# Performance work log

Hardware: AMD Instinct MI355X
Metric: run time of the kernel (lower is better)

Reference implementation:

```python
import jax, jax.numpy as jnp
import numpy as np
import math

B, T, EMB, HD = 4, 2048, 2048, 128
HALF = HD // 2


def setup_inputs() -> dict:
    key = jax.random.key(0)
    ks = jax.random.split(key, 4)
    x = jax.random.normal(ks[0], (B, T, EMB), dtype=jnp.float32)
    s = 1.0 / math.sqrt(EMB)
    Wq = jax.random.normal(ks[1], (EMB, HD), dtype=jnp.float32) * s
    Wk = jax.random.normal(ks[2], (EMB, HD), dtype=jnp.float32) * s
    Wv = jax.random.normal(ks[3], (EMB, HD), dtype=jnp.float32) * s
    # Standard RoPE rotation table: theta_i = 10000^(-2i/HD), angle = pos * theta
    inv_freq = 1.0 / (10000.0 ** (np.arange(0, HALF, dtype=np.float32) / HALF))
    angles = np.arange(T, dtype=np.float32)[:, None] * inv_freq[None, :]  # [T, HALF]
    rot_cos = jnp.asarray(np.cos(angles), dtype=jnp.float32)
    rot_sin = jnp.asarray(np.sin(angles), dtype=jnp.float32)
    # Additive causal mask: 0 on/below diagonal, -1e9 above
    NEG = -1e9
    mask = jnp.where(jnp.tril(jnp.ones((T, T), dtype=bool)), 0.0, NEG).astype(jnp.float32)
    return {"x": x, "Wq": Wq, "Wk": Wk, "Wv": Wv,
            "rot_cos": rot_cos, "rot_sin": rot_sin, "mask": mask}


def _apply_rope(q, rot_cos, rot_sin):
    # q: [B, T, HD]; view last dim as HALF complex pairs and rotate
    qp = q.reshape(q.shape[0], q.shape[1], HALF, 2)
    re, im = qp[..., 0], qp[..., 1]
    out_re = re * rot_cos - im * rot_sin  # broadcast [T,HALF] over batch
    out_im = re * rot_sin + im * rot_cos
    return jnp.stack([out_re, out_im], axis=-1).reshape(q.shape)


def reference(x, Wq, Wk, Wv, rot_cos, rot_sin, mask):
    Q = x @ Wq  # [B, T, HD]
    K = x @ Wk
    V = x @ Wv
    Q = _apply_rope(Q, rot_cos, rot_sin)
    K = _apply_rope(K, rot_cos, rot_sin)
    scores = jnp.einsum('bqd,bkd->bqk', Q, K) / math.sqrt(HD)
    probs = jax.nn.softmax(scores + mask, axis=-1)  # dropout is identity in eval
    return jnp.einsum('bqk,bkd->bqd', probs, V)
```

## Files before the change

kernel.cpp:

```cpp
#include <hip/hip_runtime.h>
#include <cstddef>
#include <cstdint>

#define T_SEQ 2048
#define EMB_D 2048
#define HD_D  128

typedef __attribute__((ext_vector_type(8))) short short8;
typedef __attribute__((ext_vector_type(4))) float f32x4;
typedef __attribute__((ext_vector_type(4))) unsigned short ushort4v;
typedef __attribute__((ext_vector_type(8))) unsigned short ushort8v;
typedef __attribute__((ext_vector_type(2))) unsigned int uint2v;

static __device__ __forceinline__ unsigned short f2bf_rne(float f) {
    union { float f; unsigned u; } v; v.f = f;
    unsigned r = v.u + 0x7fffu + ((v.u >> 16) & 1u);
    return (unsigned short)(r >> 16);
}
static __device__ __forceinline__ unsigned short f2bf_fast(float f) {
    union { float f; unsigned u; } v; v.f = f;
    return (unsigned short)((v.u + 0x8000u) >> 16);
}
static __device__ __forceinline__ float bf2f(unsigned short h) {
    union { unsigned u; float f; } v; v.u = ((unsigned)h) << 16;
    return v.f;
}
static __device__ __forceinline__ unsigned pk2(float a, float b) {
    union { float f; unsigned u; } x, y; x.f = a; y.f = b;
    return __builtin_amdgcn_perm(y.u + 0x8000u, x.u + 0x8000u, 0x07060302);
}
#define EXP2F(x) __builtin_amdgcn_exp2f(x)

__global__ __launch_bounds__(256) void prep_weights(
    const float* __restrict__ Wq, const float* __restrict__ Wk,
    const float* __restrict__ Wv, unsigned short* __restrict__ Wt)
{
    __shared__ __attribute__((aligned(16))) unsigned short tw[64 * 132];
    const int w = blockIdx.y;
    const int k0 = blockIdx.x * 64;
    const float* W = (w == 0) ? Wq : (w == 1) ? Wk : Wv;
    const int tid = threadIdx.x;
#pragma unroll
    for (int p = 0; p < 8; p++) {
        const int f = p * 256 + tid;
        const int row = f >> 5, c4 = f & 31;
        const float4 v = *(const float4*)&W[(size_t)(k0 + row) * HD_D + c4 * 4];
        ushort4v h = { f2bf_rne(v.x), f2bf_rne(v.y), f2bf_rne(v.z), f2bf_rne(v.w) };
        *(ushort4v*)&tw[row * 132 + c4 * 4] = h;
    }
    __syncthreads();
    const int kk = (tid & 7) * 8;
#pragma unroll
    for (int p = 0; p < 4; p++) {
        const int n = p * 32 + (tid >> 3);
        ushort8v o;
#pragma unroll
        for (int jj = 0; jj < 8; jj++) o[jj] = tw[(kk + jj) * 132 + n];
        *(ushort8v*)&Wt[(size_t)w * (HD_D * EMB_D) + (size_t)n * EMB_D + k0 + kk] = o;
    }
}

__global__ __launch_bounds__(256, 4) void qkv_fused(
    const float* __restrict__ x, const unsigned short* __restrict__ Wt,
    const float* __restrict__ rcos, const float* __restrict__ rsin,
    unsigned short* __restrict__ Qb, unsigned short* __restrict__ Kb,
    unsigned short* __restrict__ Vt)
{
    __shared__ __attribute__((aligned(16))) unsigned short xsm[2][32 * 64];
    __shared__ __attribute__((aligned(16))) unsigned short wsm[2][96 * 64];
    const int L = blockIdx.x;
    const int xcd = L & 7, s = L >> 3;
    const int ng = s & 3;
    const int m0 = (xcd * 32 + (s >> 2)) * 32;
    const int tid = threadIdx.x;
    const int lane = tid & 63, wave = tid >> 6;
    const int wm = wave >> 1, wn = wave & 1;
    const int l15 = lane & 15, lq = lane >> 4;

    const int xrow = tid >> 4, xc = tid & 15;
    const float* xsrc = x + (size_t)(m0 + xrow) * EMB_D + xc * 4;
    const int wrow = tid >> 3, wc = tid & 7;
    const unsigned short* wsrc = Wt + (size_t)(ng * 96 + wrow) * EMB_D + wc * 8;

    const int xw  = xrow * 128 + (((xc >> 1) ^ (xrow & 7)) << 4) + (xc & 1) * 8;
    const int wwo = wrow * 128 + ((wc ^ (wrow & 7)) << 4);

    int ra[2], rb[3][2];
#pragma unroll
    for (int ks = 0; ks < 2; ks++) {
        const int row = wm * 16 + l15;
        ra[ks] = row * 128 + (((ks * 4 + lq) ^ (row & 7)) << 4);
    }
#pragma unroll
    for (int jj = 0; jj < 3; jj++)
#pragma unroll
        for (int ks = 0; ks < 2; ks++) {
            const int row = wn * 48 + jj * 16 + l15;
            rb[jj][ks] = row * 128 + (((ks * 4 + lq) ^ (row & 7)) << 4);
        }

    f32x4 acc[3];
#pragma unroll
    for (int j = 0; j < 3; j++) acc[j] = (f32x4){0.f, 0.f, 0.f, 0.f};

    float4 xr[2][2];
    short8 wr[2][3];

#define LOADN(SET, K)                                                             \
    do {                                                                          \
        _Pragma("unroll")                                                         \
        for (int p = 0; p < 2; p++)                                               \
            xr[SET][p] = *(const float4*)(xsrc + (size_t)p * (16 * EMB_D) + (K)); \
        _Pragma("unroll")                                                         \
        for (int p = 0; p < 3; p++)                                               \
            wr[SET][p] = *(const short8*)(wsrc + (size_t)p * (32 * EMB_D) + (K)); \
    } while (0)

#define STAGE(SET, BUF)                                                           \
    do {                                                                          \
        char* xb = (char*)&xsm[BUF][0];                                           \
        char* wb = (char*)&wsm[BUF][0];                                           \
        _Pragma("unroll")                                                         \
        for (int p = 0; p < 2; p++) {                                             \
            uint2v u;                                                             \
            u.x = pk2(xr[SET][p].x, xr[SET][p].y);                                \
            u.y = pk2(xr[SET][p].z, xr[SET][p].w);                                \
            *(uint2v*)(xb + xw + p * 2048) = u;                                   \
        }                                                                         \
        _Pragma("unroll")                                                         \
        for (int p = 0; p < 3; p++)                                               \
            *(short8*)(wb + wwo + p * 4096) = wr[SET][p];                         \
    } while (0)

#define COMPUTE(BUF)                                                              \
    do {                                                                          \
        const char* xb = (const char*)&xsm[BUF][0];                               \
        const char* wb = (const char*)&wsm[BUF][0];                               \
        short8 Af[2];                                                             \
        _Pragma("unroll")                                                         \
        for (int ks = 0; ks < 2; ks++)                                            \
            Af[ks] = *(const short8*)(xb + ra[ks]);                               \
        __builtin_amdgcn_s_setprio(1);                                            \
        _Pragma("unroll")                                                         \
        for (int ks = 0; ks < 2; ks++)                                            \
            _Pragma("unroll")                                                     \
            for (int jj = 0; jj < 3; jj++) {                                      \
                const short8 Bf = *(const short8*)(wb + rb[jj][ks]);              \
                acc[jj] = __builtin_amdgcn_mfma_f32_16x16x32_bf16(                \
                    Af[ks], Bf, acc[jj], 0, 0, 0);                                \
            }                                                                     \
        __builtin_amdgcn_s_setprio(0);                                            \
    } while (0)

#define BARX() asm volatile("s_waitcnt lgkmcnt(0)\n\ts_barrier" ::: "memory")

    LOADN(0, 0);
    LOADN(1, 64);
    STAGE(0, 0);
    LOADN(0, 128);

#pragma clang loop unroll(disable)
    for (int j = 0; j < 28; j += 2) {
        BARX(); STAGE(1, 1); LOADN(1, (j + 3) * 64); COMPUTE(0);
        BARX(); STAGE(0, 0); LOADN(0, (j + 4) * 64); COMPUTE(1);
    }
    BARX(); STAGE(1, 1); LOADN(1, 31 * 64); COMPUTE(0);
    BARX(); STAGE(0, 0);                    COMPUTE(1);
    BARX(); STAGE(1, 1);                    COMPUTE(0);
    BARX();                                 COMPUTE(1);

#undef LOADN
#undef STAGE
#undef COMPUTE
#undef BARX

    const float qscale = 0.08838834764831845f * 1.4426950408889634f;
#pragma unroll
    for (int r = 0; r < 4; r++) {
        const int row = m0 + wm * 16 + lq * 4 + r;
        const int t = row & (T_SEQ - 1);
        const int bb = row >> 11;
#pragma unroll
        for (int j = 0; j < 3; j++) {
            const int col = ng * 96 + wn * 48 + j * 16 + l15;
            const int mat = col >> 7, mcol = col & 127;
            const float v = acc[j][r];
            if (mat == 2) {
                Vt[((size_t)bb * HD_D + mcol) * T_SEQ + t] = f2bf_rne(v);
            } else {
                const int ip = mcol >> 1;
                const float c = rcos[t * 64 + ip];
                const float s2 = rsin[t * 64 + ip];
                const float pv = __shfl_xor(v, 1);
                float rv = (mcol & 1) ? (pv * s2 + v * c) : (v * c - pv * s2);
                if (mat == 0) {
                    rv *= qscale;
                    Qb[(size_t)row * HD_D + mcol] = f2bf_rne(rv);
                } else {
                    Kb[(size_t)row * HD_D + mcol] = f2bf_rne(rv);
                }
            }
        }
    }
}

__global__ __launch_bounds__(256, 2) void attn(
    const unsigned short* __restrict__ Qb, const unsigned short* __restrict__ Kb,
    const unsigned short* __restrict__ Vt, float* __restrict__ O0,
    unsigned short* __restrict__ O1, float* __restrict__ Lp)
{
    __shared__ __attribute__((aligned(16))) unsigned short O_s[4][16 * 128];
    __shared__ __attribute__((aligned(16))) unsigned short P_s[4][2][16 * 40];
    __shared__ float l_s[4][16];

    const int tid = threadIdx.x;
    const int lane = tid & 63, wave = tid >> 6;
    const int l15 = lane & 15, lq = lane >> 4;
    const int kf = lq * 8;

    const int L = blockIdx.x;
    const int g = L & 1;
    const int b = (L >> 1) & 3;
    const int q0 = (127 - (L >> 3)) * 16;
    const int kend = q0 + 16;
    const float M2 = 16.0f;

    const unsigned short* Qp = Qb + (size_t)(b * T_SEQ + q0) * HD_D;
    short8 aQ[4];
#pragma unroll
    for (int d = 0; d < 4; d++)
        aQ[d] = *(const short8*)&Qp[l15 * HD_D + d * 32 + kf];

    f32x4 acc[8];
#pragma unroll
    for (int d = 0; d < 8; d++) acc[d] = (f32x4){0.f, 0.f, 0.f, 0.f};
    float l_r[4] = {0.f, 0.f, 0.f, 0.f};

    const unsigned short* Kbase = Kb + (size_t)b * T_SEQ * HD_D;
    const unsigned short* Vbase = Vt + (size_t)b * HD_D * T_SEQ;
    unsigned short* PwA = &P_s[wave][0][0];
    unsigned short* PwB = &P_s[wave][1][0];

    for (int c = 2 * wave + g; c * 32 < kend; c += 16) {
        const int kA = c * 32;
        const int kB = (c + 8) * 32;
        const bool hB = kB < kend;

        const unsigned short* KpA = Kbase + (size_t)kA * HD_D;
        const unsigned short* KpB = Kbase + (size_t)kB * HD_D;
        short8 KA[8], KB_[8];
#pragma unroll
        for (int d = 0; d < 4; d++)
#pragma unroll
            for (int n = 0; n < 2; n++)
                KA[d * 2 + n] = *(const short8*)&KpA[(size_t)(n * 16 + l15) * HD_D + d * 32 + kf];
        if (hB) {
#pragma unroll
            for (int d = 0; d < 4; d++)
#pragma unroll
                for (int n = 0; n < 2; n++)
                    KB_[d * 2 + n] = *(const short8*)&KpB[(size_t)(n * 16 + l15) * HD_D + d * 32 + kf];
        }

        f32x4 sA0 = (f32x4){0.f, 0.f, 0.f, 0.f}, sA1 = sA0, sB0 = sA0, sB1 = sA0;
#pragma unroll
        for (int d = 0; d < 4; d++) {
            sA0 = __builtin_amdgcn_mfma_f32_16x16x32_bf16(aQ[d], KA[d * 2 + 0], sA0, 0, 0, 0);
            sA1 = __builtin_amdgcn_mfma_f32_16x16x32_bf16(aQ[d], KA[d * 2 + 1], sA1, 0, 0, 0);
        }
        if (hB) {
#pragma unroll
            for (int d = 0; d < 4; d++) {
                sB0 = __builtin_amdgcn_mfma_f32_16x16x32_bf16(aQ[d], KB_[d * 2 + 0], sB0, 0, 0, 0);
                sB1 = __builtin_amdgcn_mfma_f32_16x16x32_bf16(aQ[d], KB_[d * 2 + 1], sB1, 0, 0, 0);
            }
        }

        short8 VA[8];
#pragma unroll
        for (int d = 0; d < 8; d++)
            VA[d] = *(const short8*)&Vbase[(size_t)(d * 16 + l15) * T_SEQ + kA + kf];

#pragma unroll
        for (int r = 0; r < 4; r++) {
            const int q = q0 + lq * 4 + r;
            const float p0 = ((kA + l15)      <= q) ? EXP2F(sA0[r] - M2) : 0.f;
            const float p1 = ((kA + 16 + l15) <= q) ? EXP2F(sA1[r] - M2) : 0.f;
            l_r[r] += p0 + p1;
            const int prow = (lq * 4 + r) * 40;
            PwA[prow + l15]      = f2bf_fast(p0);
            PwA[prow + 16 + l15] = f2bf_fast(p1);
        }
        const short8 pA = *(const short8*)&PwA[l15 * 40 + kf];
#pragma unroll
        for (int d = 0; d < 8; d++)
            acc[d] = __builtin_amdgcn_mfma_f32_16x16x32_bf16(pA, VA[d], acc[d], 0, 0, 0);

        if (hB) {
            short8 VB[8];
#pragma unroll
            for (int d = 0; d < 8; d++)
                VB[d] = *(const short8*)&Vbase[(size_t)(d * 16 + l15) * T_SEQ + kB + kf];
#pragma unroll
            for (int r = 0; r < 4; r++) {
                const int q = q0 + lq * 4 + r;
                const float p0 = ((kB + l15)      <= q) ? EXP2F(sB0[r] - M2) : 0.f;
                const float p1 = ((kB + 16 + l15) <= q) ? EXP2F(sB1[r] - M2) : 0.f;
                l_r[r] += p0 + p1;
                const int prow = (lq * 4 + r) * 40;
                PwB[prow + l15]      = f2bf_fast(p0);
                PwB[prow + 16 + l15] = f2bf_fast(p1);
            }
            const short8 pB = *(const short8*)&PwB[l15 * 40 + kf];
#pragma unroll
            for (int d = 0; d < 8; d++)
                acc[d] = __builtin_amdgcn_mfma_f32_16x16x32_bf16(pB, VB[d], acc[d], 0, 0, 0);
        }
    }

#pragma unroll
    for (int r = 0; r < 4; r++) {
        float lr = l_r[r];
        lr += __shfl_xor(lr, 1);
        lr += __shfl_xor(lr, 2);
        lr += __shfl_xor(lr, 4);
        lr += __shfl_xor(lr, 8);
        if (l15 == 0) l_s[wave][lq * 4 + r] = lr;
#pragma unroll
        for (int d = 0; d < 8; d++)
            O_s[wave][(lq * 4 + r) * 128 + d * 16 + l15] = f2bf_fast(acc[d][r]);
    }
    __syncthreads();

    const int row = tid >> 4;
    const int dc = (tid & 15) * 8;
    const float lt = l_s[0][row] + l_s[1][row] + l_s[2][row] + l_s[3][row];
    float o[8];
#pragma unroll
    for (int k = 0; k < 8; k++) o[k] = 0.f;
#pragma unroll
    for (int w2 = 0; w2 < 4; w2++) {
        const ushort8v pv = *(const ushort8v*)&O_s[w2][row * 128 + dc];
#pragma unroll
        for (int k = 0; k < 8; k++) o[k] += bf2f(pv[k]);
    }
    const size_t grow = (size_t)(b * T_SEQ + q0 + row);
    if (g == 0) {
        float* op = O0 + grow * HD_D + dc;
#pragma unroll
        for (int k = 0; k < 8; k++) op[k] = o[k];
    } else {
        ushort8v h;
#pragma unroll
        for (int k = 0; k < 8; k++) h[k] = f2bf_fast(o[k]);
        *(ushort8v*)&O1[grow * HD_D + dc] = h;
    }
    if ((tid & 15) == 0) Lp[g * 8192 + grow] = lt;
}

__global__ __launch_bounds__(256) void attn_merge(
    float* __restrict__ out, const unsigned short* __restrict__ O1,
    const float* __restrict__ Lp)
{
    const int idx = blockIdx.x * 256 + threadIdx.x;
    const int row = idx >> 5;
    f32x4 a = ((f32x4*)out)[idx];
    const ushort4v h = ((const ushort4v*)O1)[idx];
    f32x4 bv = { bf2f(h.x), bf2f(h.y), bf2f(h.z), bf2f(h.w) };
    const float inv = 1.0f / (Lp[row] + Lp[8192 + row]);
    ((f32x4*)out)[idx] = (a + bv) * inv;
}

extern "C" void kernel_launch(void* const* d_in, const int* in_sizes, int n_in,
                              void* d_out, int out_size, void* d_ws, size_t ws_size,
                              hipStream_t stream)
{
    (void)in_sizes; (void)n_in; (void)out_size; (void)ws_size;
    const float* x  = (const float*)d_in[0];
    const float* Wq = (const float*)d_in[1];
    const float* Wk = (const float*)d_in[2];
    const float* Wv = (const float*)d_in[3];
    const float* rc = (const float*)d_in[4];
    const float* rs = (const float*)d_in[5];
    float* out = (float*)d_out;

    char* ws = (char*)d_ws;
    unsigned short* Wt = (unsigned short*)(ws);
    unsigned short* Qb = (unsigned short*)(ws + 1572864);
    unsigned short* Kb = (unsigned short*)(ws + 3670016);
    unsigned short* Vt = (unsigned short*)(ws + 5767168);
    unsigned short* O1 = (unsigned short*)(ws + 7864320);
    float*          Lp = (float*)(ws + 9961472);

    prep_weights<<<dim3(32, 3), 256, 0, stream>>>(Wq, Wk, Wv, Wt);
    qkv_fused   <<<dim3(1024),  256, 0, stream>>>(x, Wt, rc, rs, Qb, Kb, Vt);
    attn        <<<dim3(1024),  256, 0, stream>>>(Qb, Kb, Vt, out, O1, Lp);
    attn_merge  <<<dim3(1024),  256, 0, stream>>>(out, O1, Lp);
}
```

Measured before the change: 187.7 us.

## Enlarge QKV projection and attention tiles to raise per-block data reuse

The QKV projection kernel moves to 512-thread blocks, each covering 192 output columns (half of QKV) instead of 96, with a three-register-set load pipeline. The attention kernel now processes 32 query rows per block instead of 16, so every K/V tile loaded is reused across two Q sub-tiles. Grids are halved for both kernels. This cuts redundant global loads of x and K/V, at the cost of fewer blocks, more registers and more shared memory per block, and less parallelism for short causal rows.

Measured after the change: 173.5 us. 7.6% less time.

```diff
diff --git a/kernel.cpp b/kernel.cpp
--- a/kernel.cpp
+++ b/kernel.cpp
@@ -60,27 +60,27 @@
     }
 }
 
-__global__ __launch_bounds__(256, 4) void qkv_fused(
+__global__ __launch_bounds__(512, 4) void qkv_fused(
     const float* __restrict__ x, const unsigned short* __restrict__ Wt,
     const float* __restrict__ rcos, const float* __restrict__ rsin,
     unsigned short* __restrict__ Qb, unsigned short* __restrict__ Kb,
     unsigned short* __restrict__ Vt)
 {
     __shared__ __attribute__((aligned(16))) unsigned short xsm[2][32 * 64];
-    __shared__ __attribute__((aligned(16))) unsigned short wsm[2][96 * 64];
+    __shared__ __attribute__((aligned(16))) unsigned short wsm[2][192 * 64];
     const int L = blockIdx.x;
     const int xcd = L & 7, s = L >> 3;
-    const int ng = s & 3;
-    const int m0 = (xcd * 32 + (s >> 2)) * 32;
+    const int cg = s & 1;
+    const int m0 = (xcd * 32 + (s >> 1)) * 32;
     const int tid = threadIdx.x;
     const int lane = tid & 63, wave = tid >> 6;
-    const int wm = wave >> 1, wn = wave & 1;
+    const int wm = wave >> 2, wn = wave & 3;
     const int l15 = lane & 15, lq = lane >> 4;
 
     const int xrow = tid >> 4, xc = tid & 15;
     const float* xsrc = x + (size_t)(m0 + xrow) * EMB_D + xc * 4;
     const int wrow = tid >> 3, wc = tid & 7;
-    const unsigned short* wsrc = Wt + (size_t)(ng * 96 + wrow) * EMB_D + wc * 8;
+    const unsigned short* wsrc = Wt + (size_t)(cg * 192 + wrow) * EMB_D + wc * 8;
 
     const int xw  = xrow * 128 + (((xc >> 1) ^ (xrow & 7)) << 4) + (xc & 1) * 8;
     const int wwo = wrow * 128 + ((wc ^ (wrow & 7)) << 4);
@@ -103,33 +103,28 @@
 #pragma unroll
     for (int j = 0; j < 3; j++) acc[j] = (f32x4){0.f, 0.f, 0.f, 0.f};
 
-    float4 xr[2][2];
-    short8 wr[2][3];
+    float4 xr[3];
+    short8 wr[3][3];
 
 #define LOADN(SET, K)                                                             \
     do {                                                                          \
-        _Pragma("unroll")                                                         \
-        for (int p = 0; p < 2; p++)                                               \
-            xr[SET][p] = *(const float4*)(xsrc + (size_t)p * (16 * EMB_D) + (K)); \
+        xr[SET] = *(const float4*)(xsrc + (K));                                   \
         _Pragma("unroll")                                                         \
         for (int p = 0; p < 3; p++)                                               \
-            wr[SET][p] = *(const short8*)(wsrc + (size_t)p * (32 * EMB_D) + (K)); \
+            wr[SET][p] = *(const short8*)(wsrc + (size_t)p * (64 * EMB_D) + (K)); \
     } while (0)
 
 #define STAGE(SET, BUF)                                                           \
     do {                                                                          \
         char* xb = (char*)&xsm[BUF][0];                                           \
         char* wb = (char*)&wsm[BUF][0];                                           \
-        _Pragma("unroll")                                                         \
-        for (int p = 0; p < 2; p++) {                                             \
-            uint2v u;                                                             \
-            u.x = pk2(xr[SET][p].x, xr[SET][p].y);                                \
-            u.y = pk2(xr[SET][p].z, xr[SET][p].w);                                \
-            *(uint2v*)(xb + xw + p * 2048) = u;                                   \
-        }                                                                         \
+        uint2v u;                                                                 \
+        u.x = pk2(xr[SET].x, xr[SET].y);                                          \
+        u.y = pk2(xr[SET].z, xr[SET].w);                                          \
+        *(uint2v*)(xb + xw) = u;                                                  \
         _Pragma("unroll")                                                         \
         for (int p = 0; p < 3; p++)                                               \
-            *(short8*)(wb + wwo + p * 4096) = wr[SET][p];                         \
+            *(short8*)(wb + wwo + p * 8192) = wr[SET][p];                         \
     } while (0)
 
 #define COMPUTE(BUF)                                                              \
@@ -156,15 +151,24 @@
 
     LOADN(0, 0);
     LOADN(1, 64);
+    LOADN(2, 128);
     STAGE(0, 0);
-    LOADN(0, 128);
+    LOADN(0, 192);
 
 #pragma clang loop unroll(disable)
-    for (int j = 0; j < 28; j += 2) {
-        BARX(); STAGE(1, 1); LOADN(1, (j + 3) * 64); COMPUTE(0);
-        BARX(); STAGE(0, 0); LOADN(0, (j + 4) * 64); COMPUTE(1);
-    }
-    BARX(); STAGE(1, 1); LOADN(1, 31 * 64); COMPUTE(0);
+    for (int j = 0; j < 24; j += 6) {
+        BARX(); STAGE(1, 1); LOADN(1, (j + 4) * 64); COMPUTE(0);
+        BARX(); STAGE(2, 0); LOADN(2, (j + 5) * 64); COMPUTE(1);
+        BARX(); STAGE(0, 1); LOADN(0, (j + 6) * 64); COMPUTE(0);
+        BARX(); STAGE(1, 0); LOADN(1, (j + 7) * 64); COMPUTE(1);
+        BARX(); STAGE(2, 1); LOADN(2, (j + 8) * 64); COMPUTE(0);
+        BARX(); STAGE(0, 0); LOADN(0, (j + 9) * 64); COMPUTE(1);
+    }
+    BARX(); STAGE(1, 1); LOADN(1, 28 * 64); COMPUTE(0);
+    BARX(); STAGE(2, 0); LOADN(2, 29 * 64); COMPUTE(1);
+    BARX(); STAGE(0, 1); LOADN(0, 30 * 64); COMPUTE(0);
+    BARX(); STAGE(1, 0); LOADN(1, 31 * 64); COMPUTE(1);
+    BARX(); STAGE(2, 1);                    COMPUTE(0);
     BARX(); STAGE(0, 0);                    COMPUTE(1);
     BARX(); STAGE(1, 1);                    COMPUTE(0);
     BARX();                                 COMPUTE(1);
@@ -182,7 +186,7 @@
         const int bb = row >> 11;
 #pragma unroll
         for (int j = 0; j < 3; j++) {
-            const int col = ng * 96 + wn * 48 + j * 16 + l15;
+            const int col = cg * 192 + wn * 48 + j * 16 + l15;
             const int mat = col >> 7, mcol = col & 127;
             const float v = acc[j][r];
             if (mat == 2) {
@@ -209,9 +213,9 @@
     const unsigned short* __restrict__ Vt, float* __restrict__ O0,
     unsigned short* __restrict__ O1, float* __restrict__ Lp)
 {
-    __shared__ __attribute__((aligned(16))) unsigned short O_s[4][16 * 128];
-    __shared__ __attribute__((aligned(16))) unsigned short P_s[4][2][16 * 40];
-    __shared__ float l_s[4][16];
+    __shared__ __attribute__((aligned(16))) unsigned short O_s[4][32 * 128];
+    __shared__ __attribute__((aligned(16))) unsigned short P_s[4][32 * 40];
+    __shared__ float l_s[4][32];
 
     const int tid = threadIdx.x;
     const int lane = tid & 63, wave = tid >> 6;
@@ -221,60 +225,52 @@
     const int L = blockIdx.x;
     const int g = L & 1;
     const int b = (L >> 1) & 3;
-    const int q0 = (127 - (L >> 3)) * 16;
-    const int kend = q0 + 16;
+    const int q0 = (63 - (L >> 3)) * 32;
+    const int kend = q0 + 32;
     const float M2 = 16.0f;
 
     const unsigned short* Qp = Qb + (size_t)(b * T_SEQ + q0) * HD_D;
-    short8 aQ[4];
-#pragma unroll
-    for (int d = 0; d < 4; d++)
-        aQ[d] = *(const short8*)&Qp[l15 * HD_D + d * 32 + kf];
-
-    f32x4 acc[8];
-#pragma unroll
-    for (int d = 0; d < 8; d++) acc[d] = (f32x4){0.f, 0.f, 0.f, 0.f};
-    float l_r[4] = {0.f, 0.f, 0.f, 0.f};
+    short8 aQ[2][4];
+#pragma unroll
+    for (int i = 0; i < 2; i++)
+#pragma unroll
+        for (int d = 0; d < 4; d++)
+            aQ[i][d] = *(const short8*)&Qp[(size_t)(i * 16 + l15) * HD_D + d * 32 + kf];
+
+    f32x4 acc[2][8];
+#pragma unroll
+    for (int i = 0; i < 2; i++)
+#pragma unroll
+        for (int d = 0; d < 8; d++) acc[i][d] = (f32x4){0.f, 0.f, 0.f, 0.f};
+    float l_r[2][4] = {{0.f, 0.f, 0.f, 0.f}, {0.f, 0.f, 0.f, 0.f}};
 
     const unsigned short* Kbase = Kb + (size_t)b * T_SEQ * HD_D;
     const unsigned short* Vbase = Vt + (size_t)b * HD_D * T_SEQ;
-    unsigned short* PwA = &P_s[wave][0][0];
-    unsigned short* PwB = &P_s[wave][1][0];
-
-    for (int c = 2 * wave + g; c * 32 < kend; c += 16) {
+    unsigned short* Pw = &P_s[wave][0];
+
+    for (int c = 2 * wave + g; c * 32 < kend; c += 8) {
         const int kA = c * 32;
-        const int kB = (c + 8) * 32;
-        const bool hB = kB < kend;
-
-        const unsigned short* KpA = Kbase + (size_t)kA * HD_D;
-        const unsigned short* KpB = Kbase + (size_t)kB * HD_D;
-        short8 KA[8], KB_[8];
+        const unsigned short* Kp = Kbase + (size_t)kA * HD_D;
+        short8 KA[8];
 #pragma unroll
         for (int d = 0; d < 4; d++)
 #pragma unroll
             for (int n = 0; n < 2; n++)
-                KA[d * 2 + n] = *(const short8*)&KpA[(size_t)(n * 16 + l15) * HD_D + d * 32 + kf];
-        if (hB) {
-#pragma unroll
-            for (int d = 0; d < 4; d++)
+                KA[d * 2 + n] = *(const short8*)&Kp[(size_t)(n * 16 + l15) * HD_D + d * 32 + kf];
+
+        f32x4 sc[2][2];
+#pragma unroll
+        for (int i = 0; i < 2; i++)
+#pragma unroll
+            for (int n = 0; n < 2; n++) sc[i][n] = (f32x4){0.f, 0.f, 0.f, 0.f};
+#pragma unroll
+        for (int d = 0; d < 4; d++)
+#pragma unroll
+            for (int i = 0; i < 2; i++)
 #pragma unroll
                 for (int n = 0; n < 2; n++)
-                    KB_[d * 2 + n] = *(const short8*)&KpB[(size_t)(n * 16 + l15) * HD_D + d * 32 + kf];
-        }
-
-        f32x4 sA0 = (f32x4){0.f, 0.f, 0.f, 0.f}, sA1 = sA0, sB0 = sA0, sB1 = sA0;
-#pragma unroll
-        for (int d = 0; d < 4; d++) {
-            sA0 = __builtin_amdgcn_mfma_f32_16x16x32_bf16(aQ[d], KA[d * 2 + 0], sA0, 0, 0, 0);
-            sA1 = __builtin_amdgcn_mfma_f32_16x16x32_bf16(aQ[d], KA[d * 2 + 1], sA1, 0, 0, 0);
-        }
-        if (hB) {
-#pragma unroll
-            for (int d = 0; d < 4; d++) {
-                sB0 = __builtin_amdgcn_mfma_f32_16x16x32_bf16(aQ[d], KB_[d * 2 + 0], sB0, 0, 0, 0);
-                sB1 = __builtin_amdgcn_mfma_f32_16x16x32_bf16(aQ[d], KB_[d * 2 + 1], sB1, 0, 0, 0);
-            }
-        }
+                    sc[i][n] = __builtin_amdgcn_mfma_f32_16x16x32_bf16(
+                        aQ[i][d], KA[d * 2 + n], sc[i][n], 0, 0, 0);
 
         short8 VA[8];
 #pragma unroll
@@ -282,80 +278,71 @@
             VA[d] = *(const short8*)&Vbase[(size_t)(d * 16 + l15) * T_SEQ + kA + kf];
 
 #pragma unroll
+        for (int i = 0; i < 2; i++)
+#pragma unroll
+            for (int r = 0; r < 4; r++) {
+                const int q = q0 + i * 16 + lq * 4 + r;
+                const float p0 = ((kA + l15)      <= q) ? EXP2F(sc[i][0][r] - M2) : 0.f;
+                const float p1 = ((kA + 16 + l15) <= q) ? EXP2F(sc[i][1][r] - M2) : 0.f;
+                l_r[i][r] += p0 + p1;
+                const int prow = (i * 16 + lq * 4 + r) * 40;
+                Pw[prow + l15]      = f2bf_fast(p0);
+                Pw[prow + 16 + l15] = f2bf_fast(p1);
+            }
+        short8 pA[2];
+#pragma unroll
+        for (int i = 0; i < 2; i++)
+            pA[i] = *(const short8*)&Pw[(i * 16 + l15) * 40 + kf];
+#pragma unroll
+        for (int i = 0; i < 2; i++)
+#pragma unroll
+            for (int d = 0; d < 8; d++)
+                acc[i][d] = __builtin_amdgcn_mfma_f32_16x16x32_bf16(pA[i], VA[d], acc[i][d], 0, 0, 0);
+    }
+
+#pragma unroll
+    for (int i = 0; i < 2; i++)
+#pragma unroll
         for (int r = 0; r < 4; r++) {
-            const int q = q0 + lq * 4 + r;
-            const float p0 = ((kA + l15)      <= q) ? EXP2F(sA0[r] - M2) : 0.f;
-            const float p1 = ((kA + 16 + l15) <= q) ? EXP2F(sA1[r] - M2) : 0.f;
-            l_r[r] += p0 + p1;
-            const int prow = (lq * 4 + r) * 40;
-            PwA[prow + l15]      = f2bf_fast(p0);
-            PwA[prow + 16 + l15] = f2bf_fast(p1);
-        }
-        const short8 pA = *(const short8*)&PwA[l15 * 40 + kf];
-#pragma unroll
-        for (int d = 0; d < 8; d++)
-            acc[d] = __builtin_amdgcn_mfma_f32_16x16x32_bf16(pA, VA[d], acc[d], 0, 0, 0);
-
-        if (hB) {
-            short8 VB[8];
+            float lr = l_r[i][r];
+            lr += __shfl_xor(lr, 1);
+            lr += __shfl_xor(lr, 2);
+            lr += __shfl_xor(lr, 4);
+            lr += __shfl_xor(lr, 8);
+            if (l15 == 0) l_s[wave][i * 16 + lq * 4 + r] = lr;
 #pragma unroll
             for (int d = 0; d < 8; d++)
-                VB[d] = *(const short8*)&Vbase[(size_t)(d * 16 + l15) * T_SEQ + kB + kf];
-#pragma unroll
-            for (int r = 0; r < 4; r++) {
-                const int q = q0 + lq * 4 + r;
-                const float p0 = ((kB + l15)      <= q) ? EXP2F(sB0[r] - M2) : 0.f;
-                const float p1 = ((kB + 16 + l15) <= q) ? EXP2F(sB1[r] - M2) : 0.f;
-                l_r[r] += p0 + p1;
-                const int prow = (lq * 4 + r) * 40;
-                PwB[prow + l15]      = f2bf_fast(p0);
-                PwB[prow + 16 + l15] = f2bf_fast(p1);
-            }
-            const short8 pB = *(const short8*)&PwB[l15 * 40 + kf];
-#pragma unroll
-            for (int d = 0; d < 8; d++)
-                acc[d] = __builtin_amdgcn_mfma_f32_16x16x32_bf16(pB, VB[d], acc[d], 0, 0, 0);
-        }
-    }
-
-#pragma unroll
-    for (int r = 0; r < 4; r++) {
-        float lr = l_r[r];
-        lr += __shfl_xor(lr, 1);
-        lr += __shfl_xor(lr, 2);
-        lr += __shfl_xor(lr, 4);
-        lr += __shfl_xor(lr, 8);
-        if (l15 == 0) l_s[wave][lq * 4 + r] = lr;
-#pragma unroll
-        for (int d = 0; d < 8; d++)
-            O_s[wave][(lq * 4 + r) * 128 + d * 16 + l15] = f2bf_fast(acc[d][r]);
-    }
+                O_s[wave][(i * 16 + lq * 4 + r) * 128 + d * 16 + l15] = f2bf_fast(acc[i][d][r]);
+        }
     __syncthreads();
 
-    const int row = tid >> 4;
-    const int dc = (tid & 15) * 8;
-    const float lt = l_s[0][row] + l_s[1][row] + l_s[2][row] + l_s[3][row];
-    float o[8];
-#pragma unroll
-    for (int k = 0; k < 8; k++) o[k] = 0.f;
-#pragma unroll
-    for (int w2 = 0; w2 < 4; w2++) {
-        const ushort8v pv = *(const ushort8v*)&O_s[w2][row * 128 + dc];
-#pragma unroll
-        for (int k = 0; k < 8; k++) o[k] += bf2f(pv[k]);
-    }
-    const size_t grow = (size_t)(b * T_SEQ + q0 + row);
-    if (g == 0) {
-        float* op = O0 + grow * HD_D + dc;
-#pragma unroll
-        for (int k = 0; k < 8; k++) op[k] = o[k];
-    } else {
-        ushort8v h;
-#pragma unroll
-        for (int k = 0; k < 8; k++) h[k] = f2bf_fast(o[k]);
-        *(ushort8v*)&O1[grow * HD_D + dc] = h;
-    }
-    if ((tid & 15) == 0) Lp[g * 8192 + grow] = lt;
+#pragma unroll
+    for (int pass = 0; pass < 2; pass++) {
+        const int row = pass * 16 + (tid >> 4);
+        const int dc = (tid & 15) * 8;
+        const float lt = l_s[0][row] + l_s[1][row] + l_s[2][row] + l_s[3][row];
+        float o[8];
+#pragma unroll
+        for (int k = 0; k < 8; k++) o[k] = 0.f;
+#pragma unroll
+        for (int w2 = 0; w2 < 4; w2++) {
+            const ushort8v pv = *(const ushort8v*)&O_s[w2][row * 128 + dc];
+#pragma unroll
+            for (int k = 0; k < 8; k++) o[k] += bf2f(pv[k]);
+        }
+        const size_t grow = (size_t)(b * T_SEQ + q0 + row);
+        if (g == 0) {
+            float* op = O0 + grow * HD_D + dc;
+#pragma unroll
+            for (int k = 0; k < 8; k++) op[k] = o[k];
+        } else {
+            ushort8v h;
+#pragma unroll
+            for (int k = 0; k < 8; k++) h[k] = f2bf_fast(o[k]);
+            *(ushort8v*)&O1[grow * HD_D + dc] = h;
+        }
+        if ((tid & 15) == 0) Lp[g * 8192 + grow] = lt;
+    }
 }
 
 __global__ __launch_bounds__(256) void attn_merge(
@@ -393,7 +380,7 @@
     float*          Lp = (float*)(ws + 9961472);
 
     prep_weights<<<dim3(32, 3), 256, 0, stream>>>(Wq, Wk, Wv, Wt);
-    qkv_fused   <<<dim3(1024),  256, 0, stream>>>(x, Wt, rc, rs, Qb, Kb, Vt);
-    attn        <<<dim3(1024),  256, 0, stream>>>(Qb, Kb, Vt, out, O1, Lp);
+    qkv_fused   <<<dim3(512),   512, 0, stream>>>(x, Wt, rc, rs, Qb, Kb, Vt);
+    attn        <<<dim3(512),   256, 0, stream>>>(Qb, Kb, Vt, out, O1, Lp);
     attn_merge  <<<dim3(1024),  256, 0, stream>>>(out, O1, Lp);
 }
```
